# Performance work log

Measured on AMD Instinct MI355X. Metric: run time of the kernel, lower is better.

Reference implementation:

```python
import jax, jax.numpy as jnp
import numpy as np

B, T, D = 2, 2048, 1024
H = 16
HD = D // H
NE = 17  # n_edge_types + 1

def setup_inputs() -> dict:
    key = jax.random.key(0)
    ks = jax.random.split(key, 6)
    x = jax.random.normal(ks[0], (B, T, D), dtype=jnp.float32)
    graph_adj = jax.random.uniform(ks[1], (B, T, T), dtype=jnp.float32)
    edge_types = jax.random.randint(ks[2], (B, T, T), 0, NE, dtype=jnp.int32)
    Wqkv = jax.random.normal(ks[3], (D, 3 * D), dtype=jnp.float32) * (D ** -0.5)
    Wproj = jax.random.normal(ks[4], (D, D), dtype=jnp.float32) * (D ** -0.5)
    adj_bias = jnp.zeros((H,), dtype=jnp.float32)
    edge_table = jax.random.normal(ks[5], (NE, H), dtype=jnp.float32) * 0.02
    return {"x": x, "graph_adj": graph_adj, "edge_types": edge_types,
            "Wqkv": Wqkv, "Wproj": Wproj, "adj_bias": adj_bias,
            "edge_table": edge_table}

def reference(x, graph_adj, edge_types, Wqkv, Wproj, adj_bias, edge_table):
    Bc, Tc, C = x.shape
    qkv = (x @ Wqkv).reshape(Bc, Tc, 3, H, HD)
    q, k, v = qkv[:, :, 0], qkv[:, :, 1], qkv[:, :, 2]  # [B,T,H,HD]
    scale = 1.0 / jnp.sqrt(jnp.asarray(HD, dtype=x.dtype))
    # scores: [B,H,T,T]
    attn = jnp.einsum('bqhd,bkhd->bhqk', q, k) * scale
    # adjacency bias per head
    attn = attn + adj_bias[None, :, None, None] * graph_adj[:, None, :, :]
    # edge-type bias: lookup [B,T,T,H] -> [B,H,T,T]
    etype_b = edge_table[edge_types]  # [B,T,T,H]
    attn = attn + jnp.transpose(etype_b, (0, 3, 1, 2))
    # causal mask (upper triangle, diag=1)
    causal = jnp.triu(jnp.ones((Tc, Tc), dtype=bool), k=1)
    attn = jnp.where(causal[None, None, :, :], jnp.asarray(-jnp.inf, dtype=attn.dtype), attn)
    attn = jax.nn.softmax(attn, axis=-1)
    out = jnp.einsum('bhqk,bkhd->bqhd', attn, v).reshape(Bc, Tc, C)
    return out @ Wproj
```

## Files before the change

kernel.cpp:

```cpp
#include <hip/hip_runtime.h>
#include <stdint.h>

#define TT 2048
#define HH 16
#define LOG2E 1.44269504089f

typedef _Float16 f16;
typedef __attribute__((ext_vector_type(8))) _Float16 f16x8;
typedef __attribute__((ext_vector_type(4))) float f32x4;
typedef unsigned short ushort_t;

__device__ __forceinline__ void gl_lds16(const void* g, void* l){
  __builtin_amdgcn_global_load_lds(
      (__attribute__((address_space(1))) void*)(void*)g,
      (__attribute__((address_space(3))) void*)l, 16, 0, 0);
}

__device__ __forceinline__ void lds_barrier(){
  __asm__ volatile("s_waitcnt lgkmcnt(0)\n\ts_barrier" ::: "memory");
}

struct SchedT { unsigned short v[80]; };
static constexpr SchedT make_sched(){
  SchedT s{};
  int idx = 0;
  for (int size = 8; size >= 1; --size){
    for (int qt = 31; qt >= 8; --qt){
      int full = qt >> 3;
      int tail = (qt & 7) + 1;
      if (size == 8)
        for (int ci = 0; ci < full; ++ci)
          s.v[idx++] = (unsigned short)(qt | (ci << 8));
      if (tail == size)
        s.v[idx++] = (unsigned short)(qt | (full << 8));
    }
    s.v[idx++] = (unsigned short)(size - 1);
  }
  return s;
}
__constant__ SchedT SCHED = make_sched();

__device__ __forceinline__ int slot_base(int qt){
  return (qt < 16) ? 2 * (qt - 8)
       : (qt < 24) ? 16 + 3 * (qt - 16)
                   : 40 + 4 * (qt - 24);
}

__global__ __launch_bounds__(256) void cvt_f2h_kernel(const float4* __restrict__ in,
                                                      uint2* __restrict__ out, int n4){
  int i = blockIdx.x * 256 + threadIdx.x;
  if (i >= n4) return;
  float4 v = in[i];
  union { f16 h[4]; uint2 u; } o;
  o.h[0] = (f16)v.x; o.h[1] = (f16)v.y; o.h[2] = (f16)v.z; o.h[3] = (f16)v.w;
  out[i] = o.u;
}

__global__ __launch_bounds__(256) void transpose_cvt_kernel(const float* __restrict__ in,
                                                            f16* __restrict__ out, int R, int C){
  __shared__ float tile[64][65];
  int c0 = blockIdx.x * 64, r0 = blockIdx.y * 64;
  int t = threadIdx.x;
  int row = t >> 2, cs = (t & 3) << 4;
  const float4* src = (const float4*)(in + (size_t)(r0 + row) * C + c0 + cs);
  float4 a = src[0], b = src[1], c = src[2], d = src[3];
  float* tr = &tile[row][cs];
  tr[0]=a.x; tr[1]=a.y; tr[2]=a.z;  tr[3]=a.w;
  tr[4]=b.x; tr[5]=b.y; tr[6]=b.z;  tr[7]=b.w;
  tr[8]=c.x; tr[9]=c.y; tr[10]=c.z; tr[11]=c.w;
  tr[12]=d.x;tr[13]=d.y;tr[14]=d.z; tr[15]=d.w;
  __syncthreads();
  f16 tmp[16];
  #pragma unroll
  for (int j = 0; j < 16; ++j) tmp[j] = (f16)tile[cs + j][row];
  f16* dst = out + (size_t)(c0 + row) * R + r0 + cs;
  *(uint4*)dst = *(uint4*)&tmp[0];
  *(uint4*)(dst + 8) = *(uint4*)&tmp[8];
}

__global__ __launch_bounds__(256) void gemm_f16_kernel(const f16* __restrict__ A,
                                                       const f16* __restrict__ Bt,
                                                       void* __restrict__ Cout,
                                                       int M, int N, int K, int out_f32){
  __shared__ __align__(16) f16 As[128 * 32];
  __shared__ __align__(16) f16 Bs[128 * 32];
  int t = threadIdx.x;
  int w = t >> 6, lane = t & 63;
  int wm = (w >> 1) * 64, wn = (w & 1) * 64;
  int lrow = lane & 15, quad = lane >> 4;
  int bm = blockIdx.y, bn = blockIdx.x;

  f32x4 acc[4][4];
  for (int i = 0; i < 4; ++i)
    for (int j = 0; j < 4; ++j)
      for (int r = 0; r < 4; ++r) acc[i][j][r] = 0.f;

  const int nk = K >> 5;
  for (int kt = 0; kt < nk; ++kt){
    int k0 = kt << 5;
    __syncthreads();
    #pragma unroll
    for (int i = 0; i < 2; ++i){
      int c = (w << 7) + (i << 6) + lane;
      gl_lds16(A  + (size_t)((bm << 7) + (c >> 2)) * K + k0 + ((c & 3) << 3),
               As + ((w << 7) + (i << 6)) * 8);
      gl_lds16(Bt + (size_t)((bn << 7) + (c >> 2)) * K + k0 + ((c & 3) << 3),
               Bs + ((w << 7) + (i << 6)) * 8);
    }
    __syncthreads();
    f16x8 af[4], bfr[4];
    #pragma unroll
    for (int mi = 0; mi < 4; ++mi)
      af[mi] = *(const f16x8*)(As + (wm + mi * 16 + lrow) * 32 + quad * 8);
    #pragma unroll
    for (int ni = 0; ni < 4; ++ni)
      bfr[ni] = *(const f16x8*)(Bs + (wn + ni * 16 + lrow) * 32 + quad * 8);
    #pragma unroll
    for (int mi = 0; mi < 4; ++mi)
      #pragma unroll
      for (int ni = 0; ni < 4; ++ni)
        acc[mi][ni] = __builtin_amdgcn_mfma_f32_16x16x32_f16(af[mi], bfr[ni], acc[mi][ni], 0, 0, 0);
  }

  #pragma unroll
  for (int mi = 0; mi < 4; ++mi)
    #pragma unroll
    for (int ni = 0; ni < 4; ++ni)
      #pragma unroll
      for (int r = 0; r < 4; ++r){
        int row = (bm << 7) + wm + mi * 16 + quad * 4 + r;
        int col = (bn << 7) + wn + ni * 16 + lrow;
        float val = acc[mi][ni][r];
        if (out_f32) ((float*)Cout)[(size_t)row * N + col] = val;
        else         ((f16*)Cout)[(size_t)row * N + col] = (f16)val;
      }
}

__global__ __launch_bounds__(256, 4) void attn_kernel(const f16* __restrict__ qkv,
                                                      const float* __restrict__ gadj,
                                                      const int* __restrict__ etype,
                                                      const float* __restrict__ adj_bias,
                                                      const float* __restrict__ edge_table,
                                                      f16* __restrict__ attn_out,
                                                      f16* __restrict__ Opart,
                                                      float* __restrict__ MLpart){
  __shared__ __align__(16) f16 Ks[64 * 72];
  __shared__ __align__(16) f16 Vt[64 * 72];
  __shared__ __align__(16) f16 Ps[4][16 * 72];
  __shared__ float edge_lds[8 * 33];

  int bx = blockIdx.x;
  int bh = bx & 31;
  int h = bh & 15, b = bh >> 4;
  int ej = SCHED.v[bx >> 5];
  int qt = ej & 31, ci = ej >> 8;
  int ksrt = ci << 3;
  int kend = min(qt, ksrt + 7);
  bool whole = (qt < 8);

  int t = threadIdx.x;
  int w = t >> 6, lane = t & 63;
  int lrow = lane & 15, quad = lane >> 4;

  if (t < 136){
    int cp = t / 17, e = t - cp * 17;
    edge_lds[cp * 33 + e] = edge_table[e * HH + h] * LOG2E;
  }
  float adjb = adj_bias[h] * LOG2E;
  int erep = (lane & 7) * 33;

  int q0 = qt * 64 + w * 16;
  const size_t qrow = ((size_t)b * TT + q0 + lrow) * 3072 + h * 64;
  f16x8 qf0 = *(const f16x8*)(qkv + qrow + quad * 8);
  f16x8 qf1 = *(const f16x8*)(qkv + qrow + 32 + quad * 8);

  f32x4 o[4];
  for (int i = 0; i < 4; ++i)
    for (int r = 0; r < 4; ++r) o[i][r] = 0.f;
  float mrun[4] = {-1e30f, -1e30f, -1e30f, -1e30f};
  float lrun[4] = {0.f, 0.f, 0.f, 0.f};

  const int keyA = t >> 3,        hdA = (t & 7) << 3;
  const int keyB = 32 + (t >> 3), hdB = hdA;
  const int sA = ((keyA >> 3) ^ (hdA >> 3)) & 7;
  const int sB = ((keyB >> 3) ^ (hdB >> 3)) & 7;
  const f16* kbase = qkv + (size_t)b * TT * 3072 + 1024 + h * 64;
  const f16* vbase = qkv + (size_t)b * TT * 3072 + 2048 + h * 64;

  const float SCL = 0.125f * LOG2E;

  for (int kt2 = ksrt; kt2 <= kend; ++kt2){
    lds_barrier();
    uint4 kv0 = *(const uint4*)(kbase + (size_t)(kt2 * 64 + keyA) * 3072 + hdA);
    uint4 kv1 = *(const uint4*)(kbase + (size_t)(kt2 * 64 + keyB) * 3072 + hdB);
    uint4 vv0 = *(const uint4*)(vbase + (size_t)(kt2 * 64 + keyA) * 3072 + hdA);
    uint4 vv1 = *(const uint4*)(vbase + (size_t)(kt2 * 64 + keyB) * 3072 + hdB);

    int qgb = q0 + quad * 4;
    int kgb = kt2 * 64 + lrow;
    float gv[16]; int ev[16];
    #pragma unroll
    for (int nb = 0; nb < 4; ++nb){
      size_t idx0 = ((size_t)b * TT + qgb) * TT + kgb + nb * 16;
      #pragma unroll
      for (int r = 0; r < 4; ++r){
        size_t idx = idx0 + (size_t)r * TT;
        gv[nb * 4 + r] = gadj[idx];
        ev[nb * 4 + r] = etype[idx];
      }
    }

    *(uint4*)(Ks + keyA * 72 + hdA) = kv0;
    *(uint4*)(Ks + keyB * 72 + hdB) = kv1;
    {
      union { uint4 u; f16 hh[8]; } ua, ub;
      ua.u = vv0; ub.u = vv1;
      #pragma unroll
      for (int jj = 0; jj < 8; ++jj){
        Vt[(hdA + jj) * 72 + (sA << 3) + (keyA & 7)] = ua.hh[jj];
        Vt[(hdB + jj) * 72 + (sB << 3) + (keyB & 7)] = ub.hh[jj];
      }
    }
    lds_barrier();

    f32x4 sf[4];
    #pragma unroll
    for (int nb = 0; nb < 4; ++nb){
      f32x4 s = {0.f, 0.f, 0.f, 0.f};
      f16x8 kf0 = *(const f16x8*)(Ks + (nb * 16 + lrow) * 72 + quad * 8);
      f16x8 kf1 = *(const f16x8*)(Ks + (nb * 16 + lrow) * 72 + 32 + quad * 8);
      s = __builtin_amdgcn_mfma_f32_16x16x32_f16(qf0, kf0, s, 0, 0, 0);
      s = __builtin_amdgcn_mfma_f32_16x16x32_f16(qf1, kf1, s, 0, 0, 0);
      sf[nb] = s;
    }

    float sarr[4][4];
    bool diag = (kt2 == qt);
    #pragma unroll
    for (int nb = 0; nb < 4; ++nb){
      int kg = kgb + nb * 16;
      #pragma unroll
      for (int r = 0; r < 4; ++r){
        float v;
        if (diag && kg > qgb + r) v = -1e30f;
        else v = sf[nb][r] * SCL + adjb * gv[nb * 4 + r] + edge_lds[erep + ev[nb * 4 + r]];
        sarr[nb][r] = v;
      }
    }

    float mx[4];
    bool need = false;
    #pragma unroll
    for (int r = 0; r < 4; ++r){
      float m_ = fmaxf(fmaxf(sarr[0][r], sarr[1][r]), fmaxf(sarr[2][r], sarr[3][r]));
      m_ = fmaxf(m_, __shfl_xor(m_, 1));
      m_ = fmaxf(m_, __shfl_xor(m_, 2));
      m_ = fmaxf(m_, __shfl_xor(m_, 4));
      m_ = fmaxf(m_, __shfl_xor(m_, 8));
      mx[r] = m_;
      need = need || (m_ > mrun[r] + 5.0f);
    }
    if (__any(need)){
      #pragma unroll
      for (int r = 0; r < 4; ++r){
        float mnew = fmaxf(mrun[r], mx[r]);
        float alpha = exp2f(mrun[r] - mnew);
        lrun[r] *= alpha;
        #pragma unroll
        for (int nbh = 0; nbh < 4; ++nbh) o[nbh][r] *= alpha;
        mrun[r] = mnew;
      }
    }
    float pv_[4][4];
    #pragma unroll
    for (int r = 0; r < 4; ++r){
      float rs = 0.f;
      #pragma unroll
      for (int nb = 0; nb < 4; ++nb){
        float p = exp2f(sarr[nb][r] - mrun[r]);
        pv_[nb][r] = p; rs += p;
      }
      rs += __shfl_xor(rs, 1); rs += __shfl_xor(rs, 2);
      rs += __shfl_xor(rs, 4); rs += __shfl_xor(rs, 8);
      lrun[r] += rs;
    }

    f16* Pw = &Ps[w][0];
    #pragma unroll
    for (int nb = 0; nb < 4; ++nb)
      #pragma unroll
      for (int r = 0; r < 4; ++r)
        Pw[(quad * 4 + r) * 72 + nb * 16 + lrow] = (f16)pv_[nb][r];
    __asm__ volatile("s_waitcnt lgkmcnt(0)" ::: "memory");

    #pragma unroll
    for (int cc = 0; cc < 2; ++cc){
      f16x8 pf = *(const f16x8*)(Pw + lrow * 72 + cc * 32 + quad * 8);
      #pragma unroll
      for (int nbh = 0; nbh < 4; ++nbh){
        int hd = nbh * 16 + lrow;
        int sb = (hd >> 3) & 7;
        f16x8 vf = *(const f16x8*)(Vt + hd * 72 + (((cc * 4 + quad) ^ sb) << 3));
        o[nbh] = __builtin_amdgcn_mfma_f32_16x16x32_f16(pf, vf, o[nbh], 0, 0, 0);
      }
    }
  }

  if (whole){
    float inv[4];
    #pragma unroll
    for (int r = 0; r < 4; ++r) inv[r] = 1.0f / lrun[r];
    #pragma unroll
    for (int nbh = 0; nbh < 4; ++nbh)
      #pragma unroll
      for (int r = 0; r < 4; ++r){
        int qg = q0 + quad * 4 + r;
        int col = h * 64 + nbh * 16 + lrow;
        attn_out[((size_t)b * TT + qg) * 1024 + col] = (f16)(o[nbh][r] * inv[r]);
      }
  } else {
    int slot = bh * 72 + slot_base(qt) + ci;
    f16* Ob = Opart + (size_t)slot * 4096;
    #pragma unroll
    for (int nbh = 0; nbh < 4; ++nbh)
      #pragma unroll
      for (int r = 0; r < 4; ++r)
        Ob[(w * 16 + quad * 4 + r) * 64 + nbh * 16 + lrow] = (f16)o[nbh][r];
    if (lrow == 0){
      #pragma unroll
      for (int r = 0; r < 4; ++r){
        int qq = w * 16 + quad * 4 + r;
        MLpart[(size_t)slot * 128 + qq] = mrun[r];
        MLpart[(size_t)slot * 128 + 64 + qq] = lrun[r];
      }
    }
  }
}

__global__ __launch_bounds__(256) void combine_kernel(const f16* __restrict__ Opart,
                                                      const float* __restrict__ ML,
                                                      f16* __restrict__ attn_out){
  int qt = blockIdx.x + 8;
  int bh = blockIdx.y;
  int nch = (qt >> 3) + 1;
  int slot0 = bh * 72 + slot_base(qt);
  int t = threadIdx.x;
  int q = t >> 2;
  int hd0 = (t & 3) << 4;

  float m[4], l[4];
  float M = -1e30f;
  #pragma unroll
  for (int c = 0; c < 4; ++c){
    if (c < nch){
      m[c] = ML[(size_t)(slot0 + c) * 128 + q];
      l[c] = ML[(size_t)(slot0 + c) * 128 + 64 + q];
      M = fmaxf(M, m[c]);
    } else { m[c] = -1e30f; l[c] = 0.f; }
  }
  float acc[16];
  #pragma unroll
  for (int i = 0; i < 16; ++i) acc[i] = 0.f;
  float L = 0.f;
  #pragma unroll
  for (int c = 0; c < 4; ++c){
    if (c < nch){
      float wgt = exp2f(m[c] - M);
      L += l[c] * wgt;
      const f16* O = Opart + (size_t)(slot0 + c) * 4096 + q * 64 + hd0;
      f16x8 a0 = *(const f16x8*)O, a1 = *(const f16x8*)(O + 8);
      #pragma unroll
      for (int i = 0; i < 8; ++i){
        acc[i]     += (float)a0[i] * wgt;
        acc[i + 8] += (float)a1[i] * wgt;
      }
    }
  }
  float invL = 1.0f / L;
  f16 outv[16];
  #pragma unroll
  for (int i = 0; i < 16; ++i) outv[i] = (f16)(acc[i] * invL);
  int b = bh >> 4, h = bh & 15;
  f16* dst = attn_out + ((size_t)b * TT + qt * 64 + q) * 1024 + h * 64 + hd0;
  *(uint4*)dst = *(uint4*)&outv[0];
  *(uint4*)(dst + 8) = *(uint4*)&outv[8];
}

extern "C" void kernel_launch(void* const* d_in, const int* in_sizes, int n_in,
                              void* d_out, int out_size, void* d_ws, size_t ws_size,
                              hipStream_t stream){
  (void)in_sizes; (void)n_in; (void)out_size; (void)ws_size;
  const float* x_f32  = (const float*)d_in[0];
  const float* gadj   = (const float*)d_in[1];
  const int*   etype  = (const int*)d_in[2];
  const float* wqkv   = (const float*)d_in[3];
  const float* wproj  = (const float*)d_in[4];
  const float* adjb   = (const float*)d_in[5];
  const float* etab   = (const float*)d_in[6];

  char* ws = (char*)d_ws;
  f16*   x_f16  = (f16*)(ws);
  f16*   qkv    = (f16*)(ws + (8u  << 20));
  f16*   wqkvT  = (f16*)(ws + (32u << 20));
  f16*   Opart  = (f16*)(ws + (32u << 20));
  f16*   wprojT = (f16*)(ws + (51u << 20));
  float* MLpart = (float*)(ws + (53u << 20));
  f16*   attn_o = x_f16;

  cvt_f2h_kernel<<<4096, 256, 0, stream>>>((const float4*)x_f32, (uint2*)x_f16, 1048576);
  transpose_cvt_kernel<<<dim3(48, 16), 256, 0, stream>>>(wqkv, wqkvT, 1024, 3072);
  transpose_cvt_kernel<<<dim3(16, 16), 256, 0, stream>>>(wproj, wprojT, 1024, 1024);
  gemm_f16_kernel<<<dim3(24, 32), 256, 0, stream>>>(x_f16, wqkvT, qkv, 4096, 3072, 1024, 0);
  attn_kernel<<<2560, 256, 0, stream>>>(qkv, gadj, etype, adjb, etab, attn_o, Opart, MLpart);
  combine_kernel<<<dim3(24, 32), 256, 0, stream>>>(Opart, MLpart, attn_o);
  gemm_f16_kernel<<<dim3(8, 32), 256, 0, stream>>>(attn_o, wprojT, d_out, 4096, 1024, 1024, 1);
}
```

Baseline: 286.1 us.

## Prepack adjacency and edge-type bias per tile and prefetch next KV tile

```diff
diff --git a/kernel.cpp b/kernel.cpp
--- a/kernel.cpp
+++ b/kernel.cpp
@@ -54,6 +54,34 @@
   union { f16 h[4]; uint2 u; } o;
   o.h[0] = (f16)v.x; o.h[1] = (f16)v.y; o.h[2] = (f16)v.z; o.h[3] = (f16)v.w;
   out[i] = o.u;
+}
+
+__global__ __launch_bounds__(256) void pack_bias_kernel(const float* __restrict__ gadj,
+                                                        const int* __restrict__ etype,
+                                                        uint32_t* __restrict__ out){
+  int bid = blockIdx.x;
+  int b = bid / 528, ti = bid - b * 528;
+  int qt = (int)((sqrtf(8.f * (float)ti + 1.f) - 1.f) * 0.5f);
+  while ((qt + 1) * (qt + 2) / 2 <= ti) ++qt;
+  while (qt * (qt + 1) / 2 > ti) --qt;
+  int kt = ti - qt * (qt + 1) / 2;
+
+  int t = threadIdx.x;
+  int row = t >> 2, c0 = (t & 3) << 4;
+  size_t src = ((size_t)b * TT + qt * 64 + row) * TT + kt * 64 + c0;
+  uint32_t* dst = out + (size_t)bid * 4096 + row * 64 + c0;
+  #pragma unroll
+  for (int v4 = 0; v4 < 4; ++v4){
+    float4 g = *(const float4*)(gadj + src + v4 * 4);
+    int4   e = *(const int4*)(etype + src + v4 * 4);
+    union { f16 h; ushort_t u; } c;
+    uint4 o;
+    c.h = (f16)g.x; o.x = (uint32_t)c.u | ((uint32_t)e.x << 16);
+    c.h = (f16)g.y; o.y = (uint32_t)c.u | ((uint32_t)e.y << 16);
+    c.h = (f16)g.z; o.z = (uint32_t)c.u | ((uint32_t)e.z << 16);
+    c.h = (f16)g.w; o.w = (uint32_t)c.u | ((uint32_t)e.w << 16);
+    *(uint4*)(dst + v4 * 4) = o;
+  }
 }
 
 __global__ __launch_bounds__(256) void transpose_cvt_kernel(const float* __restrict__ in,
@@ -137,8 +165,7 @@
 }
 
 __global__ __launch_bounds__(256, 4) void attn_kernel(const f16* __restrict__ qkv,
-                                                      const float* __restrict__ gadj,
-                                                      const int* __restrict__ etype,
+                                                      const uint32_t* __restrict__ pbias,
                                                       const float* __restrict__ adj_bias,
                                                       const float* __restrict__ edge_table,
                                                       f16* __restrict__ attn_out,
@@ -189,38 +216,45 @@
 
   const float SCL = 0.125f * LOG2E;
 
-  for (int kt2 = ksrt; kt2 <= kend; ++kt2){
+  const int tribase = b * 528 + ((qt * (qt + 1)) >> 1);
+  const size_t rowbase = (size_t)((w * 16 + quad * 4) * 64 + lrow);
+  const int qgb = q0 + quad * 4;
+
+  uint4 ka, kb, va, vb;
+  uint32_t bA[16], bB[16];
+
+  auto issue_kv = [&](int kt){
+    const f16* kr = kbase + (size_t)(kt * 64) * 3072;
+    const f16* vr = vbase + (size_t)(kt * 64) * 3072;
+    ka = *(const uint4*)(kr + (size_t)keyA * 3072 + hdA);
+    kb = *(const uint4*)(kr + (size_t)keyB * 3072 + hdB);
+    va = *(const uint4*)(vr + (size_t)keyA * 3072 + hdA);
+    vb = *(const uint4*)(vr + (size_t)keyB * 3072 + hdB);
+  };
+  auto issue_bias = [&](int kt, uint32_t (&bd)[16]){
+    const uint32_t* tp = pbias + (size_t)(tribase + kt) * 4096 + rowbase;
+    #pragma unroll
+    for (int nb = 0; nb < 4; ++nb)
+      #pragma unroll
+      for (int r = 0; r < 4; ++r)
+        bd[nb * 4 + r] = tp[(size_t)r * 64 + nb * 16];
+  };
+
+  auto process = [&](int kt2, uint32_t (&bc)[16], uint32_t (&bn)[16]){
+    __asm__ volatile("s_waitcnt vmcnt(0)" ::: "memory");
     lds_barrier();
-    uint4 kv0 = *(const uint4*)(kbase + (size_t)(kt2 * 64 + keyA) * 3072 + hdA);
-    uint4 kv1 = *(const uint4*)(kbase + (size_t)(kt2 * 64 + keyB) * 3072 + hdB);
-    uint4 vv0 = *(const uint4*)(vbase + (size_t)(kt2 * 64 + keyA) * 3072 + hdA);
-    uint4 vv1 = *(const uint4*)(vbase + (size_t)(kt2 * 64 + keyB) * 3072 + hdB);
-
-    int qgb = q0 + quad * 4;
-    int kgb = kt2 * 64 + lrow;
-    float gv[16]; int ev[16];
-    #pragma unroll
-    for (int nb = 0; nb < 4; ++nb){
-      size_t idx0 = ((size_t)b * TT + qgb) * TT + kgb + nb * 16;
-      #pragma unroll
-      for (int r = 0; r < 4; ++r){
-        size_t idx = idx0 + (size_t)r * TT;
-        gv[nb * 4 + r] = gadj[idx];
-        ev[nb * 4 + r] = etype[idx];
-      }
-    }
-
-    *(uint4*)(Ks + keyA * 72 + hdA) = kv0;
-    *(uint4*)(Ks + keyB * 72 + hdB) = kv1;
+    *(uint4*)(Ks + keyA * 72 + hdA) = ka;
+    *(uint4*)(Ks + keyB * 72 + hdB) = kb;
     {
       union { uint4 u; f16 hh[8]; } ua, ub;
-      ua.u = vv0; ub.u = vv1;
+      ua.u = va; ub.u = vb;
       #pragma unroll
       for (int jj = 0; jj < 8; ++jj){
         Vt[(hdA + jj) * 72 + (sA << 3) + (keyA & 7)] = ua.hh[jj];
         Vt[(hdB + jj) * 72 + (sB << 3) + (keyB & 7)] = ub.hh[jj];
       }
     }
+    if (kt2 < kend){ issue_kv(kt2 + 1); issue_bias(kt2 + 1, bn); }
     lds_barrier();
 
     f32x4 sf[4];
@@ -234,6 +268,7 @@
       sf[nb] = s;
     }
 
+    int kgb = kt2 * 64 + lrow;
     float sarr[4][4];
     bool diag = (kt2 == qt);
     #pragma unroll
@@ -243,7 +278,11 @@
       for (int r = 0; r < 4; ++r){
         float v;
         if (diag && kg > qgb + r) v = -1e30f;
-        else v = sf[nb][r] * SCL + adjb * gv[nb * 4 + r] + edge_lds[erep + ev[nb * 4 + r]];
+        else {
+          uint32_t bp = bc[nb * 4 + r];
+          union { ushort_t u; f16 h; } cv; cv.u = (ushort_t)bp;
+          v = sf[nb][r] * SCL + adjb * (float)cv.h + edge_lds[erep + (bp >> 16)];
+        }
         sarr[nb][r] = v;
       }
     }
@@ -304,6 +343,14 @@
         o[nbh] = __builtin_amdgcn_mfma_f32_16x16x32_f16(pf, vf, o[nbh], 0, 0, 0);
       }
     }
+  };
+
+  issue_kv(ksrt); issue_bias(ksrt, bA);
+  for (int kt2 = ksrt; ; ){
+    process(kt2, bA, bB);
+    if (++kt2 > kend) break;
+    process(kt2, bB, bA);
+    if (++kt2 > kend) break;
   }
 
   if (whole){
@@ -399,19 +446,21 @@
   const float* etab   = (const float*)d_in[6];
 
   char* ws = (char*)d_ws;
-  f16*   x_f16  = (f16*)(ws);
-  f16*   qkv    = (f16*)(ws + (8u  << 20));
-  f16*   wqkvT  = (f16*)(ws + (32u << 20));
-  f16*   Opart  = (f16*)(ws + (32u << 20));
-  f16*   wprojT = (f16*)(ws + (51u << 20));
-  float* MLpart = (float*)(ws + (53u << 20));
-  f16*   attn_o = x_f16;
+  f16*     x_f16  = (f16*)(ws);
+  f16*     qkv    = (f16*)(ws + (8u  << 20));
+  f16*     wqkvT  = (f16*)(ws + (32u << 20));
+  f16*     Opart  = (f16*)(ws + (32u << 20));
+  f16*     wprojT = (f16*)(ws + (51u << 20));
+  float*   MLpart = (float*)(ws + (53u << 20));
+  uint32_t* pbias = (uint32_t*)(ws + (55u << 20));
+  f16*     attn_o = x_f16;
 
   cvt_f2h_kernel<<<4096, 256, 0, stream>>>((const float4*)x_f32, (uint2*)x_f16, 1048576);
+  pack_bias_kernel<<<1056, 256, 0, stream>>>(gadj, etype, pbias);
   transpose_cvt_kernel<<<dim3(48, 16), 256, 0, stream>>>(wqkv, wqkvT, 1024, 3072);
   transpose_cvt_kernel<<<dim3(16, 16), 256, 0, stream>>>(wproj, wprojT, 1024, 1024);
   gemm_f16_kernel<<<dim3(24, 32), 256, 0, stream>>>(x_f16, wqkvT, qkv, 4096, 3072, 1024, 0);
-  attn_kernel<<<2560, 256, 0, stream>>>(qkv, gadj, etype, adjb, etab, attn_o, Opart, MLpart);
+  attn_kernel<<<2560, 256, 0, stream>>>(qkv, pbias, adjb, etab, attn_o, Opart, MLpart);
   combine_kernel<<<dim3(24, 32), 256, 0, stream>>>(Opart, MLpart, attn_o);
   gemm_f16_kernel<<<dim3(8, 32), 256, 0, stream>>>(attn_o, wprojT, d_out, 4096, 1024, 1024, 1);
 }
```

Result: slower. 357.6 us (+25.0%).
